# Kernel tuning notes

Measured on AMD Instinct MI355X. Metric: run time of the kernel, lower is better.

Reference implementation:

```python
import jax, jax.numpy as jnp
import numpy as np

HEADS = 4
DIM_HEAD = 32
SCALE = 10.0
EPS = 1e-12  # F.normalize eps


def setup_inputs() -> dict:
    key = jax.random.key(0)
    k0, k1, k2 = jax.random.split(key, 3)
    b, c, h, w = 4, 256, 64, 64
    hidden = HEADS * DIM_HEAD  # 128
    x = jax.random.normal(k0, (b, c, h, w), dtype=jnp.float32)
    # 1x1 convs == per-pixel linear layers; store as [out_ch, in_ch]
    w_qkv = jax.random.normal(k1, (3 * hidden, c), dtype=jnp.float32) * (1.0 / np.sqrt(c))
    w_out = jax.random.normal(k2, (c, hidden), dtype=jnp.float32) * (1.0 / np.sqrt(hidden))
    b_out = jnp.zeros((c,), dtype=jnp.float32)
    return {"x": x, "w_qkv": w_qkv, "w_out": w_out, "b_out": b_out}


def _l2norm(t):
    # normalize along the per-head feature dim d (axis=2 of [b,h,d,n])
    n = jnp.sqrt(jnp.sum(t * t, axis=2, keepdims=True))
    return t / jnp.maximum(n, EPS)


def reference(x, w_qkv, w_out, b_out):
    b, c, h, w = x.shape
    n = h * w
    # to_qkv 1x1 conv (no bias)
    qkv = jnp.einsum('oc,bchw->bohw', w_qkv, x)          # [b, 3*hidden, h, w]
    qkv = qkv.reshape(b, 3, HEADS, DIM_HEAD, n)          # chunk dim=1 then split heads
    q, k, v = qkv[:, 0], qkv[:, 1], qkv[:, 2]            # each [b, heads, d, n]
    q = _l2norm(q)
    k = _l2norm(k)
    sim = jnp.einsum('bhdi,bhdj->bhij', q, k) * SCALE    # [b, heads, n, n]
    attn = jax.nn.softmax(sim, axis=-1)
    out = jnp.einsum('bhij,bhdj->bhid', attn, v)         # [b, heads, n, d]
    # 'b h (x y) d -> b (h d) x y'
    out = out.transpose(0, 1, 3, 2).reshape(b, HEADS * DIM_HEAD, h, w)
    # to_out 1x1 conv with bias
    return jnp.einsum('oc,bchw->bohw', w_out, out) + b_out[None, :, None, None]
```

## Files before the change

### kernel.cpp

```cpp
#include <hip/hip_runtime.h>
#include <math.h>

#define BB 4
#define CC 256
#define NHEAD 4
#define DH 32
#define NN 4096
#define HID 128

typedef _Float16 f16;
typedef _Float16 f16x8 __attribute__((ext_vector_type(8)));
typedef _Float16 f16x4 __attribute__((ext_vector_type(4)));
typedef float f32x4 __attribute__((ext_vector_type(4)));

#define QPRESCALE 14.42695041f
#define NSHIFT 14.42695041f

#if __has_builtin(__builtin_amdgcn_exp2f)
#define EXP2F(x) __builtin_amdgcn_exp2f(x)
#else
#define EXP2F(x) __expf((x)*0.6931471805599453f)
#endif

__device__ __forceinline__ f16x8 cvt8(const float* p) {
    float4 a = *(const float4*)p;
    float4 b = *(const float4*)(p + 4);
    f16x8 r;
    r[0] = (f16)a.x; r[1] = (f16)a.y; r[2] = (f16)a.z; r[3] = (f16)a.w;
    r[4] = (f16)b.x; r[5] = (f16)b.y; r[6] = (f16)b.z; r[7] = (f16)b.w;
    return r;
}

__global__ __launch_bounds__(256) void qkv_fused(const float* __restrict__ x,
                                                 const float* __restrict__ wq,
                                                 f16* __restrict__ qh,
                                                 f16* __restrict__ kh,
                                                 f16* __restrict__ vh) {
    int wave = threadIdx.x >> 6, lane = threadIdx.x & 63;
    int quad = lane >> 4, col = lane & 15;
    int b = blockIdx.z;
    int o0 = blockIdx.y * 64;
    int i0 = blockIdx.x * 128 + wave * 32;
    const float* xb = x + (size_t)b * CC * NN;

    f32x4 c[4][2];
#pragma unroll
    for (int mt = 0; mt < 4; mt++)
#pragma unroll
        for (int nt = 0; nt < 2; nt++) c[mt][nt] = f32x4{0.f, 0.f, 0.f, 0.f};

#pragma unroll
    for (int k0 = 0; k0 < CC; k0 += 32) {
        f16x8 a[4];
#pragma unroll
        for (int mt = 0; mt < 4; mt++)
            a[mt] = cvt8(wq + (size_t)(o0 + mt * 16 + col) * CC + k0 + quad * 8);
#pragma unroll
        for (int nt = 0; nt < 2; nt++) {
            const float* xc = xb + (size_t)(k0 + quad * 8) * NN + i0 + nt * 16 + col;
            f16x8 bf;
#pragma unroll
            for (int j = 0; j < 8; j++) bf[j] = (f16)xc[(size_t)j * NN];
#pragma unroll
            for (int mt = 0; mt < 4; mt++)
                c[mt][nt] = __builtin_amdgcn_mfma_f32_16x16x32_f16(a[mt], bf, c[mt][nt], 0, 0, 0);
        }
    }

    if (o0 < 256) {
        int isQ = (o0 < 128);
        int obase = isQ ? o0 : (o0 - 128);
        f16* dst = isQ ? qh : kh;
        float pre = isQ ? QPRESCALE : 1.0f;
#pragma unroll
        for (int nt = 0; nt < 2; nt++) {
#pragma unroll
            for (int hh = 0; hh < 2; hh++) {
                float ss = 0.f;
#pragma unroll
                for (int m2 = 0; m2 < 2; m2++)
#pragma unroll
                    for (int r = 0; r < 4; r++) {
                        float v = c[hh * 2 + m2][nt][r];
                        ss = fmaf(v, v, ss);
                    }
                ss += __shfl_xor(ss, 16);
                ss += __shfl_xor(ss, 32);
                float inv = pre / fmaxf(sqrtf(ss), 1e-12f);
                int h = (obase + hh * 32) >> 5;
                size_t row = ((size_t)(b * 4 + h) * NN + i0 + nt * 16 + col) * 32;
#pragma unroll
                for (int m2 = 0; m2 < 2; m2++) {
                    f16x4 st;
#pragma unroll
                    for (int r = 0; r < 4; r++) st[r] = (f16)(c[hh * 2 + m2][nt][r] * inv);
                    *(f16x4*)(dst + row + m2 * 16 + quad * 4) = st;
                }
            }
        }
    } else {
        int o2 = o0 - 256;
#pragma unroll
        for (int nt = 0; nt < 2; nt++) {
            int i = i0 + nt * 16 + col;
#pragma unroll
            for (int mt = 0; mt < 4; mt++) {
                int h = (o2 + mt * 16) >> 5;
                int d = (mt & 1) * 16 + quad * 4;
#pragma unroll
                for (int r = 0; r < 4; r++)
                    vh[((size_t)(b * 4 + h) * 32 + d + r) * NN + i] = (f16)c[mt][nt][r];
            }
        }
    }
}

#define KROW 40
#define VROW 72

struct KV32 {
    f16x8 k0, k1;
    f16x4 v0n0, v0n1, v1n0, v1n1;
};

__device__ __forceinline__ KV32 lds_frags(const f16* kl, const f16* vl,
                                          int jb, int col, int quad) {
    KV32 f;
    f.k0 = *(const f16x8*)(kl + (jb + col) * KROW + quad * 8);
    f.k1 = *(const f16x8*)(kl + (jb + 16 + col) * KROW + quad * 8);
    f.v0n0 = *(const f16x4*)(vl + col * VROW + jb + quad * 4);
    f.v0n1 = *(const f16x4*)(vl + (16 + col) * VROW + jb + quad * 4);
    f.v1n0 = *(const f16x4*)(vl + col * VROW + jb + 16 + quad * 4);
    f.v1n1 = *(const f16x4*)(vl + (16 + col) * VROW + jb + 16 + quad * 4);
    return f;
}

__device__ __forceinline__ f16x4 expblk(f32x4 s, float& lacc) {
    float p0 = EXP2F(s[0]), p1 = EXP2F(s[1]);
    float p2 = EXP2F(s[2]), p3 = EXP2F(s[3]);
    lacc += (p0 + p1) + (p2 + p3);
    f16x4 r;
    r[0] = (f16)p0; r[1] = (f16)p1; r[2] = (f16)p2; r[3] = (f16)p3;
    return r;
}

__device__ __forceinline__ void compute32(const KV32& f, f16x8 qB0, f16x8 qB1,
                                          f32x4& o00, f32x4& o01,
                                          f32x4& o10, f32x4& o11,
                                          float& l0, float& l1) {
    const f32x4 zs = {-NSHIFT, -NSHIFT, -NSHIFT, -NSHIFT};
    f32x4 s00 = __builtin_amdgcn_mfma_f32_16x16x32_f16(f.k0, qB0, zs, 0, 0, 0);
    f32x4 s10 = __builtin_amdgcn_mfma_f32_16x16x32_f16(f.k0, qB1, zs, 0, 0, 0);
    f32x4 s01 = __builtin_amdgcn_mfma_f32_16x16x32_f16(f.k1, qB0, zs, 0, 0, 0);
    f32x4 s11 = __builtin_amdgcn_mfma_f32_16x16x32_f16(f.k1, qB1, zs, 0, 0, 0);
    f16x4 p00 = expblk(s00, l0);
    f16x4 p10 = expblk(s10, l1);
    f16x4 p01 = expblk(s01, l0);
    f16x4 p11 = expblk(s11, l1);
    o00 = __builtin_amdgcn_mfma_f32_16x16x16f16(p00, f.v0n0, o00, 0, 0, 0);
    o01 = __builtin_amdgcn_mfma_f32_16x16x16f16(p00, f.v0n1, o01, 0, 0, 0);
    o10 = __builtin_amdgcn_mfma_f32_16x16x16f16(p10, f.v0n0, o10, 0, 0, 0);
    o11 = __builtin_amdgcn_mfma_f32_16x16x16f16(p10, f.v0n1, o11, 0, 0, 0);
    o00 = __builtin_amdgcn_mfma_f32_16x16x16f16(p01, f.v1n0, o00, 0, 0, 0);
    o01 = __builtin_amdgcn_mfma_f32_16x16x16f16(p01, f.v1n1, o01, 0, 0, 0);
    o10 = __builtin_amdgcn_mfma_f32_16x16x16f16(p11, f.v1n0, o10, 0, 0, 0);
    o11 = __builtin_amdgcn_mfma_f32_16x16x16f16(p11, f.v1n1, o11, 0, 0, 0);
}

__global__ __launch_bounds__(256, 4) void attn_mfma(const f16* __restrict__ qh,
                                                    const f16* __restrict__ kh,
                                                    const f16* __restrict__ vh,
                                                    f16* __restrict__ att16) {
    __shared__ __align__(16) f16 klds[2][64 * KROW];
    __shared__ __align__(16) f16 vlds[2][32 * VROW];
    int t = threadIdx.x;
    int wave = t >> 6, lane = t & 63;
    int quad = lane >> 4, col = lane & 15;

    int bid = blockIdx.x;
    int xcd = bid & 7;
    int slot = bid >> 3;
    int bh = xcd * 2 + (slot >> 5);
    int i0 = (slot & 31) * 128;
    int iw = i0 + wave * 32;

    const f16* qb = qh + (size_t)bh * NN * 32;
    const f16* kb = kh + (size_t)bh * NN * 32;
    const f16* vb = vh + (size_t)bh * 32 * NN;

    f16x8 qB0 = *(const f16x8*)(qb + (size_t)(iw + col) * 32 + quad * 8);
    f16x8 qB1 = *(const f16x8*)(qb + (size_t)(iw + 16 + col) * 32 + quad * 8);

    f32x4 o00 = {0.f, 0.f, 0.f, 0.f}, o01 = o00, o10 = o00, o11 = o00;
    float l0 = 0.f, l1 = 0.f;

    int ktr = t >> 2, kts = t & 3;
    int vtr = t >> 3, vts = t & 7;

    f16x8 kr, vr;
    kr = *(const f16x8*)(kb + (size_t)(0 + ktr) * 32 + kts * 8);
    vr = *(const f16x8*)(vb + (size_t)vtr * NN + 0 + vts * 8);
    *(f16x8*)(&klds[0][0] + ktr * KROW + kts * 8) = kr;
    *(f16x8*)(&vlds[0][0] + vtr * VROW + vts * 8) = vr;
    __syncthreads();
    kr = *(const f16x8*)(kb + (size_t)(64 + ktr) * 32 + kts * 8);
    vr = *(const f16x8*)(vb + (size_t)vtr * NN + 64 + vts * 8);

    for (int tile = 0; tile < 62; tile++) {
        int buf = tile & 1;
        const f16* kl = &klds[buf][0];
        const f16* vl = &vlds[buf][0];
        KV32 f0 = lds_frags(kl, vl, 0, col, quad);
        KV32 f1 = lds_frags(kl, vl, 32, col, quad);
        compute32(f0, qB0, qB1, o00, o01, o10, o11, l0, l1);
        compute32(f1, qB0, qB1, o00, o01, o10, o11, l0, l1);
        *(f16x8*)(&klds[buf ^ 1][0] + ktr * KROW + kts * 8) = kr;
        *(f16x8*)(&vlds[buf ^ 1][0] + vtr * VROW + vts * 8) = vr;
        __syncthreads();
        int j0 = (tile + 2) * 64;
        kr = *(const f16x8*)(kb + (size_t)(j0 + ktr) * 32 + kts * 8);
        vr = *(const f16x8*)(vb + (size_t)vtr * NN + j0 + vts * 8);
    }
    {
        KV32 f0 = lds_frags(&klds[0][0], &vlds[0][0], 0, col, quad);
        KV32 f1 = lds_frags(&klds[0][0], &vlds[0][0], 32, col, quad);
        compute32(f0, qB0, qB1, o00, o01, o10, o11, l0, l1);
        compute32(f1, qB0, qB1, o00, o01, o10, o11, l0, l1);
        *(f16x8*)(&klds[1][0] + ktr * KROW + kts * 8) = kr;
        *(f16x8*)(&vlds[1][0] + vtr * VROW + vts * 8) = vr;
        __syncthreads();
    }
    {
        KV32 f0 = lds_frags(&klds[1][0], &vlds[1][0], 0, col, quad);
        KV32 f1 = lds_frags(&klds[1][0], &vlds[1][0], 32, col, quad);
        compute32(f0, qB0, qB1, o00, o01, o10, o11, l0, l1);
        compute32(f1, qB0, qB1, o00, o01, o10, o11, l0, l1);
    }

    l0 += __shfl_xor(l0, 16); l0 += __shfl_xor(l0, 32);
    l1 += __shfl_xor(l1, 16); l1 += __shfl_xor(l1, 32);

    int b = bh >> 2, h = bh & 3;
    f16* ab = att16 + (size_t)b * NN * HID + h * 32;
#pragma unroll
    for (int r = 0; r < 4; r++) {
        float inv0 = __builtin_amdgcn_rcpf(__shfl(l0, quad * 4 + r));
        float inv1 = __builtin_amdgcn_rcpf(__shfl(l1, quad * 4 + r));
        size_t row0 = (size_t)(iw + quad * 4 + r) * HID;
        size_t row1 = (size_t)(iw + 16 + quad * 4 + r) * HID;
        ab[row0 + col]      = (f16)(o00[r] * inv0);
        ab[row0 + 16 + col] = (f16)(o01[r] * inv0);
        ab[row1 + col]      = (f16)(o10[r] * inv1);
        ab[row1 + 16 + col] = (f16)(o11[r] * inv1);
    }
}

__global__ __launch_bounds__(256) void out_mfma(const f16* __restrict__ att16,
                                                const float* __restrict__ wo,
                                                const float* __restrict__ bo,
                                                float* __restrict__ out) {
    int wave = threadIdx.x >> 6, lane = threadIdx.x & 63;
    int quad = lane >> 4, col = lane & 15;
    int b = blockIdx.z;
    int i0 = (blockIdx.x * 4 + wave) * 32;
    int o0 = blockIdx.y * 64;
    const f16* ab = att16 + (size_t)b * NN * HID;

    const f32x4 z = {0.f, 0.f, 0.f, 0.f};
    f32x4 c[2][4];
#pragma unroll
    for (int it = 0; it < 2; it++)
#pragma unroll
        for (int ot = 0; ot < 4; ot++) c[it][ot] = z;

#pragma unroll
    for (int k0 = 0; k0 < HID; k0 += 32) {
        f16x8 a0 = *(const f16x8*)(ab + (size_t)(i0 + col) * HID + k0 + quad * 8);
        f16x8 a1 = *(const f16x8*)(ab + (size_t)(i0 + 16 + col) * HID + k0 + quad * 8);
#pragma unroll
        for (int ot = 0; ot < 4; ot++) {
            f16x8 bf = cvt8(wo + (size_t)(o0 + ot * 16 + col) * HID + k0 + quad * 8);
            c[0][ot] = __builtin_amdgcn_mfma_f32_16x16x32_f16(a0, bf, c[0][ot], 0, 0, 0);
            c[1][ot] = __builtin_amdgcn_mfma_f32_16x16x32_f16(a1, bf, c[1][ot], 0, 0, 0);
        }
    }

#pragma unroll
    for (int it = 0; it < 2; it++)
#pragma unroll
        for (int ot = 0; ot < 4; ot++) {
            int o = o0 + ot * 16 + col;
            float bias = bo[o];
            int i = i0 + it * 16 + quad * 4;
            float4 st = {c[it][ot][0] + bias, c[it][ot][1] + bias,
                         c[it][ot][2] + bias, c[it][ot][3] + bias};
            *(float4*)(out + ((size_t)b * CC + o) * NN + i) = st;
        }
}

extern "C" void kernel_launch(void* const* d_in, const int* in_sizes, int n_in,
                              void* d_out, int out_size, void* d_ws, size_t ws_size,
                              hipStream_t stream) {
    const float* x     = (const float*)d_in[0];
    const float* w_qkv = (const float*)d_in[1];
    const float* w_out = (const float*)d_in[2];
    const float* b_out = (const float*)d_in[3];
    float* out = (float*)d_out;

    char* ws = (char*)d_ws;
    f16* qh    = (f16*)(ws);
    f16* kh    = (f16*)(ws + (4u << 20));
    f16* vh    = (f16*)(ws + (8u << 20));
    f16* att16 = (f16*)(ws + (12u << 20));

    qkv_fused<<<dim3(NN / 128, 384 / 64, BB), 256, 0, stream>>>(x, w_qkv, qh, kh, vh);
    attn_mfma<<<dim3(512), 256, 0, stream>>>(qh, kh, vh, att16);
    out_mfma<<<dim3(NN / 128, CC / 64, BB), 256, 0, stream>>>(att16, w_out, b_out, out);
}
```

Measured before the change: 167.3 us.

## Split attention over key dimension with partial sums and combine kernel

Splits each query tile's key/value sweep into 2 or 4 chunks handled by separate blocks, raising the grid from 512 to 1024 or 2048 blocks. Each block writes unnormalized fp32 partial outputs and row sums, and a new combine kernel adds them and normalizes into the fp16 attention buffer. This works because softmax has no max subtraction here, thanks to the bounded normalized logits. The goal is better CU occupancy and load balance on the large GPU. The cost is an extra launch plus fp32 partial traffic of tens of MB, and the split path is chosen by workspace size.

After: 165.3 us. About the same (-1.2%).

```diff
diff --git a/kernel.cpp b/kernel.cpp
--- a/kernel.cpp
+++ b/kernel.cpp
@@ -167,9 +167,12 @@
     o11 = __builtin_amdgcn_mfma_f32_16x16x16f16(p11, f.v1n1, o11, 0, 0, 0);
 }
 
+template <int SPLIT>
 __global__ __launch_bounds__(256, 4) void attn_mfma(const f16* __restrict__ qh,
                                                     const f16* __restrict__ kh,
                                                     const f16* __restrict__ vh,
+                                                    float* __restrict__ op,
+                                                    float* __restrict__ lp,
                                                     f16* __restrict__ att16) {
     __shared__ __align__(16) f16 klds[2][64 * KROW];
     __shared__ __align__(16) f16 vlds[2][32 * VROW];
@@ -180,13 +183,18 @@
     int bid = blockIdx.x;
     int xcd = bid & 7;
     int slot = bid >> 3;
-    int bh = xcd * 2 + (slot >> 5);
-    int i0 = (slot & 31) * 128;
+    int bh = xcd * 2 + slot / (32 * SPLIT);
+    int rem = slot % (32 * SPLIT);
+    int s = rem >> 5;
+    int i0 = (rem & 31) * 128;
     int iw = i0 + wave * 32;
 
+    const int NT = 64 / SPLIT;
+    int kbase = s * (NN / SPLIT);
+
     const f16* qb = qh + (size_t)bh * NN * 32;
-    const f16* kb = kh + (size_t)bh * NN * 32;
-    const f16* vb = vh + (size_t)bh * 32 * NN;
+    const f16* kb = kh + (size_t)bh * NN * 32 + (size_t)kbase * 32;
+    const f16* vb = vh + (size_t)bh * 32 * NN + kbase;
 
     f16x8 qB0 = *(const f16x8*)(qb + (size_t)(iw + col) * 32 + quad * 8);
     f16x8 qB1 = *(const f16x8*)(qb + (size_t)(iw + 16 + col) * 32 + quad * 8);
@@ -206,7 +214,7 @@
     kr = *(const f16x8*)(kb + (size_t)(64 + ktr) * 32 + kts * 8);
     vr = *(const f16x8*)(vb + (size_t)vtr * NN + 64 + vts * 8);
 
-    for (int tile = 0; tile < 62; tile++) {
+    for (int tile = 0; tile < NT - 2; tile++) {
         int buf = tile & 1;
         const f16* kl = &klds[buf][0];
         const f16* vl = &vlds[buf][0];
@@ -240,19 +248,63 @@
     l0 += __shfl_xor(l0, 16); l0 += __shfl_xor(l0, 32);
     l1 += __shfl_xor(l1, 16); l1 += __shfl_xor(l1, 32);
 
+    if constexpr (SPLIT == 1) {
+        int b = bh >> 2, h = bh & 3;
+        f16* ab = att16 + (size_t)b * NN * HID + h * 32;
+#pragma unroll
+        for (int r = 0; r < 4; r++) {
+            float inv0 = __builtin_amdgcn_rcpf(__shfl(l0, quad * 4 + r));
+            float inv1 = __builtin_amdgcn_rcpf(__shfl(l1, quad * 4 + r));
+            size_t row0 = (size_t)(iw + quad * 4 + r) * HID;
+            size_t row1 = (size_t)(iw + 16 + quad * 4 + r) * HID;
+            ab[row0 + col]      = (f16)(o00[r] * inv0);
+            ab[row0 + 16 + col] = (f16)(o01[r] * inv0);
+            ab[row1 + col]      = (f16)(o10[r] * inv1);
+            ab[row1 + 16 + col] = (f16)(o11[r] * inv1);
+        }
+    } else {
+        float* ob = op + (size_t)(s * 16 + bh) * NN * 32;
+#pragma unroll
+        for (int r = 0; r < 4; r++) {
+            size_t r0 = (size_t)(iw + quad * 4 + r) * 32;
+            size_t r1 = (size_t)(iw + 16 + quad * 4 + r) * 32;
+            ob[r0 + col]      = o00[r];
+            ob[r0 + 16 + col] = o01[r];
+            ob[r1 + col]      = o10[r];
+            ob[r1 + 16 + col] = o11[r];
+        }
+        if (quad == 0) {
+            lp[(size_t)(s * 16 + bh) * NN + iw + col]      = l0;
+            lp[(size_t)(s * 16 + bh) * NN + iw + 16 + col] = l1;
+        }
+    }
+}
+
+__global__ __launch_bounds__(256) void attn_combine(const float* __restrict__ op,
+                                                    const float* __restrict__ lp,
+                                                    f16* __restrict__ att16,
+                                                    int nsplit) {
+    int gid = blockIdx.x * 256 + threadIdx.x;
+    int rowid = gid >> 3;
+    int seg = gid & 7;
+    int bh = rowid >> 12;
+    int q = rowid & 4095;
+
+    float l = 0.f;
+    f32x4 acc = {0.f, 0.f, 0.f, 0.f};
+    for (int s = 0; s < nsplit; s++) {
+        l += lp[(size_t)(s * 16 + bh) * NN + q];
+        f32x4 a = *(const f32x4*)(op + ((size_t)(s * 16 + bh) * NN + q) * 32 + seg * 4);
+        acc += a;
+    }
+    float inv = __builtin_amdgcn_rcpf(l);
     int b = bh >> 2, h = bh & 3;
-    f16* ab = att16 + (size_t)b * NN * HID + h * 32;
-#pragma unroll
-    for (int r = 0; r < 4; r++) {
-        float inv0 = __builtin_amdgcn_rcpf(__shfl(l0, quad * 4 + r));
-        float inv1 = __builtin_amdgcn_rcpf(__shfl(l1, quad * 4 + r));
-        size_t row0 = (size_t)(iw + quad * 4 + r) * HID;
-        size_t row1 = (size_t)(iw + 16 + quad * 4 + r) * HID;
-        ab[row0 + col]      = (f16)(o00[r] * inv0);
-        ab[row0 + 16 + col] = (f16)(o01[r] * inv0);
-        ab[row1 + col]      = (f16)(o10[r] * inv1);
-        ab[row1 + 16 + col] = (f16)(o11[r] * inv1);
-    }
+    f16x4 st;
+    st[0] = (f16)(acc[0] * inv);
+    st[1] = (f16)(acc[1] * inv);
+    st[2] = (f16)(acc[2] * inv);
+    st[3] = (f16)(acc[3] * inv);
+    *(f16x4*)(att16 + ((size_t)b * NN + q) * HID + h * 32 + seg * 4) = st;
 }
 
 __global__ __launch_bounds__(256) void out_mfma(const f16* __restrict__ att16,
@@ -314,6 +366,20 @@
     f16* att16 = (f16*)(ws + (12u << 20));
 
     qkv_fused<<<dim3(NN / 128, 384 / 64, BB), 256, 0, stream>>>(x, w_qkv, qh, kh, vh);
-    attn_mfma<<<dim3(512), 256, 0, stream>>>(qh, kh, vh, att16);
+
+    if (ws_size >= (50ull << 20)) {
+        float* op = (float*)(ws + (16ull << 20));
+        float* lp = (float*)(ws + (48ull << 20));
+        attn_mfma<4><<<dim3(2048), 256, 0, stream>>>(qh, kh, vh, op, lp, att16);
+        attn_combine<<<dim3(2048), 256, 0, stream>>>(op, lp, att16, 4);
+    } else if (ws_size >= (33ull << 20)) {
+        float* op = (float*)(ws + (16ull << 20));
+        float* lp = (float*)(ws + (32ull << 20));
+        attn_mfma<2><<<dim3(1024), 256, 0, stream>>>(qh, kh, vh, op, lp, att16);
+        attn_combine<<<dim3(2048), 256, 0, stream>>>(op, lp, att16, 2);
+    } else {
+        attn_mfma<1><<<dim3(512), 256, 0, stream>>>(qh, kh, vh, nullptr, nullptr, att16);
+    }
+
     out_mfma<<<dim3(NN / 128, CC / 64, BB), 256, 0, stream>>>(att16, w_out, b_out, out);
 }
```
